# Optimization experiments

Hardware: AMD Instinct MI355X
Metric: run time of the kernel (lower is better)

The kernel has to match this reference:

```python
import jax, jax.numpy as jnp
import numpy as np

D_MODEL = 1024
N_HEAD = 16
D_HEAD = 64
D_CAT = N_HEAD * D_HEAD
HD_MLP = 4096
LN_EPS = 1e-5


def setup_inputs() -> dict:
    key = jax.random.key(0)
    ks = jax.random.split(key, 12)
    bn, t = 2, 2048
    s = lambda fan_in: 1.0 / np.sqrt(fan_in)
    return {
        "x": jax.random.normal(ks[0], (bn, t, D_MODEL), dtype=jnp.float32),
        "mask": jnp.ones((bn, t), dtype=jnp.int32),
        "w_qkv": jax.random.normal(ks[1], (D_MODEL, 3 * D_CAT), dtype=jnp.float32) * s(D_MODEL),
        "w_tail": jax.random.normal(ks[2], (D_CAT, D_MODEL), dtype=jnp.float32) * s(D_CAT),
        "b_tail": jnp.zeros((D_MODEL,), dtype=jnp.float32),
        "ln1_g": jnp.ones((D_MODEL,), dtype=jnp.float32),
        "ln1_b": jnp.zeros((D_MODEL,), dtype=jnp.float32),
        "ln2_g": jnp.ones((D_MODEL,), dtype=jnp.float32),
        "ln2_b": jnp.zeros((D_MODEL,), dtype=jnp.float32),
        "w1": jax.random.normal(ks[3], (D_MODEL, HD_MLP), dtype=jnp.float32) * s(D_MODEL),
        "b1": jnp.zeros((HD_MLP,), dtype=jnp.float32),
        "w2": jax.random.normal(ks[4], (HD_MLP, D_MODEL), dtype=jnp.float32) * s(HD_MLP),
        "b2": jnp.zeros((D_MODEL,), dtype=jnp.float32),
    }


def _layer_norm(x, g, b):
    mu = jnp.mean(x, axis=-1, keepdims=True)
    var = jnp.mean(jnp.square(x - mu), axis=-1, keepdims=True)
    return (x - mu) * jax.lax.rsqrt(var + LN_EPS) * g + b


def _attention(z, mask, w_qkv, w_tail, b_tail):
    bn, t, _ = z.shape
    qkv = z @ w_qkv                      # (bn, t, 3*d_cat)
    qkv = qkv.reshape(bn, t, N_HEAD, 3, D_HEAD)  # chunk layout: per-head [q|k|v]
    q = qkv[..., 0, :].transpose(0, 2, 1, 3)     # (bn, h, t, dh)
    k = qkv[..., 1, :].transpose(0, 2, 1, 3)
    v = qkv[..., 2, :].transpose(0, 2, 1, 3)
    scale = D_HEAD ** -0.5
    dots = jnp.einsum("bhqd,bhkd->bhqk", q, k) * scale
    key_mask = (mask == 0)[:, None, None, :]     # (bn,1,1,t)
    dots = jnp.where(key_mask, -jnp.inf, dots)
    coef = jax.nn.softmax(dots, axis=-1)
    attn = jnp.einsum("bhqk,bhkd->bhqd", coef, v)
    out = attn.transpose(0, 2, 1, 3).reshape(bn, t, D_CAT)
    return out @ w_tail + b_tail


def reference(x, mask, w_qkv, w_tail, b_tail, ln1_g, ln1_b, ln2_g, ln2_b, w1, b1, w2, b2):
    z = _layer_norm(x, ln1_g, ln1_b)
    x = _attention(z, mask, w_qkv, w_tail, b_tail) + x
    z = _layer_norm(x, ln2_g, ln2_b)
    h = jax.nn.gelu(z @ w1 + b1, approximate=False)  # torch GELU default = exact erf
    x = h @ w2 + b2 + x
    return x
```

## Files before the change

kernel.cpp:

```cpp
#include <hip/hip_runtime.h>
#include <hip/hip_bf16.h>

#define DM 1024
#define TT 2048
#define NH 16
#define DH 64
#define HD 4096

typedef __attribute__((ext_vector_type(4))) float f32x4;
typedef __attribute__((ext_vector_type(8))) short s16x8;
typedef __attribute__((ext_vector_type(4))) short s16x4;

static __device__ __forceinline__ short f2bf(float f) {
  __hip_bfloat16 h = __float2bfloat16(f);
  return *reinterpret_cast<short*>(&h);
}

typedef const __attribute__((address_space(1))) char* gas1_t;
typedef __attribute__((address_space(3))) char* las3_t;
static __device__ __forceinline__ void glds16(const void* g, void* l) {
  __builtin_amdgcn_global_load_lds((gas1_t)g, (las3_t)l, 16, 0, 0);
}

__global__ __launch_bounds__(256) void transpose_cvt_k(
    const float* __restrict__ in, short* __restrict__ out, int K, int N)
{
  __shared__ float tile[32][33];
  const int n0 = blockIdx.x * 32, k0 = blockIdx.y * 32;
  const int tx = threadIdx.x & 31, ty = threadIdx.x >> 5;
#pragma unroll
  for (int i = 0; i < 4; ++i)
    tile[ty + i * 8][tx] = in[(size_t)(k0 + ty + i * 8) * N + n0 + tx];
  __syncthreads();
#pragma unroll
  for (int i = 0; i < 4; ++i) {
    int n = ty + i * 8;
    out[(size_t)(n0 + n) * K + k0 + tx] = f2bf(tile[tx][n]);
  }
}

__global__ __launch_bounds__(256) void ln_k(
    const float* __restrict__ x, const float* __restrict__ g,
    const float* __restrict__ b, short* __restrict__ out)
{
  const int row = blockIdx.x;
  const int tid = threadIdx.x;
  const float4 v = ((const float4*)(x + (size_t)row * DM))[tid];
  float s = v.x + v.y + v.z + v.w;
  float q = v.x * v.x + v.y * v.y + v.z * v.z + v.w * v.w;
#pragma unroll
  for (int off = 1; off < 64; off <<= 1) {
    s += __shfl_xor(s, off);
    q += __shfl_xor(q, off);
  }
  __shared__ float ss[4], sq[4];
  const int wave = tid >> 6;
  if ((tid & 63) == 0) { ss[wave] = s; sq[wave] = q; }
  __syncthreads();
  s = ss[0] + ss[1] + ss[2] + ss[3];
  q = sq[0] + sq[1] + sq[2] + sq[3];
  const float mu = s * (1.0f / DM);
  const float var = q * (1.0f / DM) - mu * mu;
  const float rs = rsqrtf(var + 1e-5f);
  const float4 gv = ((const float4*)g)[tid];
  const float4 bv = ((const float4*)b)[tid];
  s16x4 o;
  o[0] = f2bf((v.x - mu) * rs * gv.x + bv.x);
  o[1] = f2bf((v.y - mu) * rs * gv.y + bv.y);
  o[2] = f2bf((v.z - mu) * rs * gv.z + bv.z);
  o[3] = f2bf((v.w - mu) * rs * gv.w + bv.w);
  *(s16x4*)(out + (size_t)row * DM + tid * 4) = o;
}

template<int EPI, int BN>
__global__ __launch_bounds__(256) void gemm_bt(
    const short* __restrict__ A, const short* __restrict__ B,
    const float* __restrict__ bias, const float* __restrict__ res,
    float* __restrict__ outF, short* __restrict__ outB,
    short* __restrict__ outK, short* __restrict__ outV,
    int M, int N, int K)
{
  constexpr int MR = (BN == 128) ? 4 : 2;
  __shared__ short As[2][128 * 32];
  __shared__ short Bs[2][BN * 32];
  const int tid = threadIdx.x;
  const int wave = tid >> 6, lane = tid & 63;
  const int l15 = lane & 15, lhi = lane >> 4;
  const int bm = blockIdx.x, bn = blockIdx.y;
  const int wr = (BN == 128) ? (wave >> 1) : wave;
  const int wc = (BN == 128) ? (wave & 1) : 0;
  f32x4 acc[MR][4] = {};

  const int sr = wave * 16 + (lane >> 2);
  const int schunk = ((lane & 3) ^ ((lane >> 3) & 3)) * 16;
  const char* gA = (const char*)(A + (size_t)(bm * 128 + sr) * K) + schunk;
  const char* gB = (const char*)(B + (size_t)(bn * BN + sr) * K) + schunk;
  const size_t rowstep = (size_t)64 * K * 2;

  const int NK = K >> 5;
  const int rsw = (l15 >> 1) & 3;
  const int achunk = (lhi ^ rsw) << 4;

  auto stage = [&](int buf, int kt) {
    const size_t koff = (size_t)kt * 64;
    char* lA = (char*)As[buf] + wave * 1024;
    glds16(gA + koff, lA);
    glds16(gA + koff + rowstep, lA + 4096);
    char* lB = (char*)Bs[buf] + wave * 1024;
    glds16(gB + koff, lB);
    if (BN == 128) glds16(gB + koff + rowstep, lB + 4096);
  };

  stage(0, 0);
  __syncthreads();
  int cur = 0;
  for (int kt = 0; kt < NK; ++kt) {
    if (kt + 1 < NK) stage(cur ^ 1, kt + 1);
    s16x8 af[MR], bfv[4];
#pragma unroll
    for (int m = 0; m < MR; ++m) {
      const int row = wr * (MR * 16) + m * 16 + l15;
      af[m] = *(const s16x8*)((const char*)As[cur] + row * 64 + achunk);
    }
#pragma unroll
    for (int n = 0; n < 4; ++n) {
      const int row = wc * 64 + n * 16 + l15;
      bfv[n] = *(const s16x8*)((const char*)Bs[cur] + row * 64 + achunk);
    }
#pragma unroll
    for (int m = 0; m < MR; ++m)
#pragma unroll
      for (int n = 0; n < 4; ++n)
        acc[m][n] = __builtin_amdgcn_mfma_f32_16x16x32_bf16(af[m], bfv[n], acc[m][n], 0, 0, 0);
    __syncthreads();
    cur ^= 1;
  }

  const int rowb = bm * 128 + wr * (MR * 16);
  const int colb = bn * BN + wc * 64;
#pragma unroll
  for (int m = 0; m < MR; ++m) {
#pragma unroll
    for (int n = 0; n < 4; ++n) {
      if (EPI == 3) {
        const int col0 = colb + n * 16;
        const int h = col0 / 192;
        const int c0 = col0 - h * 192;
        const int region = c0 >> 6;
        const int d = (c0 & 63) + l15;
        const int row0 = rowb + m * 16 + lhi * 4;
        const int bb = row0 >> 11, tl0 = row0 & 2047;
        const size_t bh = (size_t)bb * NH + h;
        if (region == 2) {
          s16x4 pk;
#pragma unroll
          for (int rr = 0; rr < 4; ++rr) pk[rr] = f2bf(acc[m][n][rr]);
          *(s16x4*)(outV + (bh * 64 + d) * TT + tl0) = pk;
        } else {
          short* dst = (region == 0) ? outB : outK;
#pragma unroll
          for (int rr = 0; rr < 4; ++rr)
            dst[(bh * TT + tl0 + rr) * 64 + d] = f2bf(acc[m][n][rr]);
        }
      } else {
        const int col = colb + n * 16 + l15;
        const float bv = bias[col];
#pragma unroll
        for (int rr = 0; rr < 4; ++rr) {
          const int row = rowb + m * 16 + lhi * 4 + rr;
          float v = acc[m][n][rr] + bv;
          if (EPI == 1) v += res[(size_t)row * N + col];
          if (EPI == 2) v = 0.5f * v * (1.0f + erff(v * 0.70710678118f));
          if (EPI == 1) outF[(size_t)row * N + col] = v;
          else outB[(size_t)row * N + col] = f2bf(v);
        }
      }
    }
  }
}

__global__ __launch_bounds__(256) void attn_k(
    const short* __restrict__ Qb, const short* __restrict__ Kb,
    const short* __restrict__ Vtb, const int* __restrict__ mask,
    short* __restrict__ outp)
{
  const int tid = threadIdx.x, wave = tid >> 6, lane = tid & 63;
  const int l15 = lane & 15, lhi = lane >> 4;
  const int bh = blockIdx.y;
  const int b = bh >> 4, h = bh & 15;
  const int q0 = blockIdx.x * 64;

  __shared__ short Ks[64 * 64];
  __shared__ short Vt[64 * 64];
  __shared__ short Ps[4][16 * 64];

  const short* qbase = Qb + ((size_t)bh * TT + q0 + wave * 16 + l15) * 64;
  const s16x8 aq0 = *(const s16x8*)(qbase + lhi * 8);
  const s16x8 aq1 = *(const s16x8*)(qbase + 32 + lhi * 8);

  f32x4 o[4] = {};
  float mrow = -1e30f, lrow = 0.f;

  const int sr = tid >> 2;
  const int tc = (tid & 3) * 16;
  const int ssw = (sr & 7) << 4;

  const short* kg0 = Kb + ((size_t)bh * TT + sr) * 64 + tc;
  const short* vg0 = Vtb + ((size_t)bh * 64 + sr) * TT + tc;
  s16x8 kr0 = *(const s16x8*)kg0, kr1 = *(const s16x8*)(kg0 + 8);
  s16x8 vr0 = *(const s16x8*)vg0, vr1 = *(const s16x8*)(vg0 + 8);
  int mcur = mask[b * TT + lane];

  for (int t0 = 0; t0 < TT; t0 += 64) {
    char* krow = (char*)Ks + sr * 128;
    *(s16x8*)(krow + ((tc * 2) ^ ssw)) = kr0;
    *(s16x8*)(krow + ((tc * 2 + 16) ^ ssw)) = kr1;
    char* vrow = (char*)Vt + sr * 128;
    *(s16x8*)(vrow + ((tc * 2) ^ ssw)) = vr0;
    *(s16x8*)(vrow + ((tc * 2 + 16) ^ ssw)) = vr1;
    __syncthreads();

    const unsigned long long mb = __ballot(mcur != 0);

    if (t0 + 64 < TT) {
      const short* kg = Kb + ((size_t)bh * TT + t0 + 64 + sr) * 64 + tc;
      const short* vg = Vtb + ((size_t)bh * 64 + sr) * TT + t0 + 64 + tc;
      kr0 = *(const s16x8*)kg; kr1 = *(const s16x8*)(kg + 8);
      vr0 = *(const s16x8*)vg; vr1 = *(const s16x8*)(vg + 8);
      mcur = mask[b * TT + t0 + 64 + lane];
    }

    f32x4 sv[4];
#pragma unroll
    for (int n = 0; n < 4; ++n) {
      const int row = n * 16 + l15;
      const int sw = (row & 7) << 4;
      const char* kr = (const char*)Ks + row * 128;
      const s16x8 a0 = *(const s16x8*)(kr + ((lhi * 16) ^ sw));
      const s16x8 a1 = *(const s16x8*)(kr + ((64 + lhi * 16) ^ sw));
      f32x4 z = {};
      z = __builtin_amdgcn_mfma_f32_16x16x32_bf16(a0, aq0, z, 0, 0, 0);
      z = __builtin_amdgcn_mfma_f32_16x16x32_bf16(a1, aq1, z, 0, 0, 0);
      sv[n] = z;
    }

    float pvv[4][4];
    float mx = -3e38f;
#pragma unroll
    for (int n = 0; n < 4; ++n) {
      const unsigned mnib = (unsigned)(mb >> (n * 16 + lhi * 4)) & 0xF;
#pragma unroll
      for (int r = 0; r < 4; ++r) {
        float val = sv[n][r] * 0.125f;
        if (!((mnib >> r) & 1)) val = -3e38f;
        pvv[n][r] = val;
        mx = fmaxf(mx, val);
      }
    }
    mx = fmaxf(mx, __shfl_xor(mx, 16));
    mx = fmaxf(mx, __shfl_xor(mx, 32));
    const float mn = fmaxf(mrow, mx);
    const float alpha = __expf(mrow - mn);
    mrow = mn;
    float sum = 0.f;
#pragma unroll
    for (int n = 0; n < 4; ++n)
#pragma unroll
      for (int r = 0; r < 4; ++r) {
        const float p = __expf(pvv[n][r] - mn);
        pvv[n][r] = p;
        sum += p;
      }
    sum += __shfl_xor(sum, 16);
    sum += __shfl_xor(sum, 32);
    lrow = lrow * alpha + sum;

    float ar[4];
#pragma unroll
    for (int rr = 0; rr < 4; ++rr) ar[rr] = __shfl(alpha, lhi * 4 + rr);
#pragma unroll
    for (int db = 0; db < 4; ++db)
#pragma unroll
      for (int rr = 0; rr < 4; ++rr) o[db][rr] *= ar[rr];

    char* pbase = (char*)Ps + wave * 2048 + l15 * 128;
    const int swp = (l15 & 7) << 4;
#pragma unroll
    for (int n = 0; n < 4; ++n) {
      s16x4 pk;
#pragma unroll
      for (int r = 0; r < 4; ++r) pk[r] = f2bf(pvv[n][r]);
      *(s16x4*)(pbase + ((n * 32 + lhi * 8) ^ swp)) = pk;
    }
    asm volatile("s_waitcnt lgkmcnt(0)" ::: "memory");
    __builtin_amdgcn_sched_barrier(0);
    const s16x8 ap0 = *(const s16x8*)(pbase + ((lhi * 16) ^ swp));
    const s16x8 ap1 = *(const s16x8*)(pbase + ((64 + lhi * 16) ^ swp));
#pragma unroll
    for (int db = 0; db < 4; ++db) {
      const int vrw = db * 16 + l15;
      const int swv = (vrw & 7) << 4;
      const char* vr = (const char*)Vt + vrw * 128;
      const s16x8 b0 = *(const s16x8*)(vr + ((lhi * 16) ^ swv));
      const s16x8 b1 = *(const s16x8*)(vr + ((64 + lhi * 16) ^ swv));
      o[db] = __builtin_amdgcn_mfma_f32_16x16x32_bf16(ap0, b0, o[db], 0, 0, 0);
      o[db] = __builtin_amdgcn_mfma_f32_16x16x32_bf16(ap1, b1, o[db], 0, 0, 0);
    }
    __syncthreads();
  }

  float lr[4];
#pragma unroll
  for (int rr = 0; rr < 4; ++rr) lr[rr] = __shfl(lrow, lhi * 4 + rr);
#pragma unroll
  for (int db = 0; db < 4; ++db) {
#pragma unroll
    for (int rr = 0; rr < 4; ++rr) {
      const int qg = q0 + wave * 16 + lhi * 4 + rr;
      const int cg = h * 64 + db * 16 + l15;
      outp[(size_t)(b * TT + qg) * DM + cg] = f2bf(o[db][rr] / lr[rr]);
    }
  }
}

extern "C" void kernel_launch(void* const* d_in, const int* in_sizes, int n_in,
                              void* d_out, int out_size, void* d_ws, size_t ws_size,
                              hipStream_t stream)
{
  const float* x      = (const float*)d_in[0];
  const int*   mask   = (const int*)d_in[1];
  const float* w_qkv  = (const float*)d_in[2];
  const float* w_tail = (const float*)d_in[3];
  const float* b_tail = (const float*)d_in[4];
  const float* ln1g   = (const float*)d_in[5];
  const float* ln1b   = (const float*)d_in[6];
  const float* ln2g   = (const float*)d_in[7];
  const float* ln2b   = (const float*)d_in[8];
  const float* w1     = (const float*)d_in[9];
  const float* b1     = (const float*)d_in[10];
  const float* w2     = (const float*)d_in[11];
  const float* b2     = (const float*)d_in[12];

  char* ws = (char*)d_ws;
  size_t off = 0;
  auto take = [&](size_t bytes) {
    char* p = ws + off;
    off += (bytes + 255) & ~(size_t)255;
    return p;
  };
  short* slotW = (short*)take((size_t)4096 * 2048 * 2);
  short* slotZ = (short*)take((size_t)4096 * 1024 * 2);
  short* qb    = (short*)take((size_t)32 * 2048 * 64 * 2);
  short* kb    = (short*)take((size_t)32 * 2048 * 64 * 2);
  short* vtb   = (short*)take((size_t)32 * 64 * 2048 * 2);
  float* x1    = (float*)take((size_t)4096 * 1024 * 4);
  short* hbuf  = (short*)take((size_t)4096 * 4096 * 2);

  transpose_cvt_k<<<dim3(3072 / 32, 1024 / 32), 256, 0, stream>>>(w_qkv, slotW, 1024, 3072);
  ln_k<<<4096, 256, 0, stream>>>(x, ln1g, ln1b, slotZ);
  gemm_bt<3, 128><<<dim3(32, 24), 256, 0, stream>>>(slotZ, slotW, nullptr, nullptr,
                                                    nullptr, qb, kb, vtb, 4096, 3072, 1024);
  attn_k<<<dim3(32, 32), 256, 0, stream>>>(qb, kb, vtb, mask, slotZ);
  transpose_cvt_k<<<dim3(1024 / 32, 1024 / 32), 256, 0, stream>>>(w_tail, slotW, 1024, 1024);
  gemm_bt<1, 64><<<dim3(32, 16), 256, 0, stream>>>(slotZ, slotW, b_tail, x,
                                                   x1, nullptr, nullptr, nullptr, 4096, 1024, 1024);
  ln_k<<<4096, 256, 0, stream>>>(x1, ln2g, ln2b, slotZ);
  transpose_cvt_k<<<dim3(4096 / 32, 1024 / 32), 256, 0, stream>>>(w1, slotW, 1024, 4096);
  gemm_bt<2, 128><<<dim3(32, 32), 256, 0, stream>>>(slotZ, slotW, b1, nullptr,
                                                    nullptr, hbuf, nullptr, nullptr, 4096, 4096, 1024);
  transpose_cvt_k<<<dim3(1024 / 32, 4096 / 32), 256, 0, stream>>>(w2, slotW, 4096, 1024);
  gemm_bt<1, 64><<<dim3(32, 16), 256, 0, stream>>>(hbuf, slotW, b2, x1,
                                                   (float*)d_out, nullptr, nullptr, nullptr, 4096, 1024, 4096);
}
```

Baseline: 299.2 us.

## Widen attention KV tile to 128, fold softmax scale into Q, lazy rescale

The QKV GEMM epilogue now multiplies Q by scale*log2(e) so attention can use exp2f without a per-element scale multiply. The attention kernel processes 128 keys per iteration with doubled shared-memory tiles. It skips mask application when all keys are valid and only rescales the running output when the row max grows by more than a threshold. Blocks are remapped onto a 1D grid to interleave batch-head pairs. The cost is more shared memory and registers per block, which may reduce occupancy, and lazy rescaling leaves exponents less tightly bounded than exact online softmax.

```diff
diff --git a/kernel.cpp b/kernel.cpp
--- a/kernel.cpp
+++ b/kernel.cpp
@@ -158,9 +158,10 @@
           *(s16x4*)(outV + (bh * 64 + d) * TT + tl0) = pk;
         } else {
           short* dst = (region == 0) ? outB : outK;
+          const float qs = (region == 0) ? 0.18033688011112042f : 1.0f;
 #pragma unroll
           for (int rr = 0; rr < 4; ++rr)
-            dst[(bh * TT + tl0 + rr) * 64 + d] = f2bf(acc[m][n][rr]);
+            dst[(bh * TT + tl0 + rr) * 64 + d] = f2bf(acc[m][n][rr] * qs);
         }
       } else {
         const int col = colb + n * 16 + l15;
@@ -186,13 +187,15 @@
 {
   const int tid = threadIdx.x, wave = tid >> 6, lane = tid & 63;
   const int l15 = lane & 15, lhi = lane >> 4;
-  const int bh = blockIdx.y;
+  const int lb = blockIdx.x;
+  const int r = lb & 31;
+  const int bh = (r & 7) * 4 + (r >> 3);
   const int b = bh >> 4, h = bh & 15;
-  const int q0 = blockIdx.x * 64;
-
-  __shared__ short Ks[64 * 64];
-  __shared__ short Vt[64 * 64];
-  __shared__ short Ps[4][16 * 64];
+  const int q0 = (lb >> 5) * 64;
+
+  __shared__ short Ks[128 * 64];
+  __shared__ short Vt[64 * 128];
+  __shared__ short Ps[4][16 * 128];
 
   const short* qbase = Qb + ((size_t)bh * TT + q0 + wave * 16 + l15) * 64;
   const s16x8 aq0 = *(const s16x8*)(qbase + lhi * 8);
@@ -201,38 +204,52 @@
   f32x4 o[4] = {};
   float mrow = -1e30f, lrow = 0.f;
 
-  const int sr = tid >> 2;
-  const int tc = (tid & 3) * 16;
-  const int ssw = (sr & 7) << 4;
-
-  const short* kg0 = Kb + ((size_t)bh * TT + sr) * 64 + tc;
-  const short* vg0 = Vtb + ((size_t)bh * 64 + sr) * TT + tc;
-  s16x8 kr0 = *(const s16x8*)kg0, kr1 = *(const s16x8*)(kg0 + 8);
-  s16x8 vr0 = *(const s16x8*)vg0, vr1 = *(const s16x8*)(vg0 + 8);
-  int mcur = mask[b * TT + lane];
-
-  for (int t0 = 0; t0 < TT; t0 += 64) {
-    char* krow = (char*)Ks + sr * 128;
-    *(s16x8*)(krow + ((tc * 2) ^ ssw)) = kr0;
-    *(s16x8*)(krow + ((tc * 2 + 16) ^ ssw)) = kr1;
-    char* vrow = (char*)Vt + sr * 128;
-    *(s16x8*)(vrow + ((tc * 2) ^ ssw)) = vr0;
-    *(s16x8*)(vrow + ((tc * 2 + 16) ^ ssw)) = vr1;
+  const int kr_s = tid >> 1, kc_s = (tid & 1) * 32;
+  const int ksw = (kr_s & 7) << 4;
+  const int vr_s = tid >> 2, vc_s = (tid & 3) * 32;
+  const int vsw = (vr_s & 7) << 4;
+
+  const short* kgb = Kb + (size_t)bh * TT * 64 + (size_t)kr_s * 64 + kc_s;
+  const short* vgb = Vtb + ((size_t)bh * 64 + vr_s) * TT + vc_s;
+
+  s16x8 kpre[4], vpre[4];
+#pragma unroll
+  for (int j = 0; j < 4; ++j) {
+    kpre[j] = *(const s16x8*)(kgb + j * 8);
+    vpre[j] = *(const s16x8*)(vgb + j * 8);
+  }
+  int m0 = mask[b * TT + lane], m1 = mask[b * TT + 64 + lane];
+
+  for (int t0 = 0; t0 < TT; t0 += 128) {
+    char* krow = (char*)Ks + kr_s * 128;
+#pragma unroll
+    for (int j = 0; j < 4; ++j)
+      *(s16x8*)(krow + ((kc_s * 2 + j * 16) ^ ksw)) = kpre[j];
+    char* vrow = (char*)Vt + vr_s * 256;
+#pragma unroll
+    for (int j = 0; j < 4; ++j)
+      *(s16x8*)(vrow + ((vc_s * 2 + j * 16) ^ vsw)) = vpre[j];
     __syncthreads();
 
-    const unsigned long long mb = __ballot(mcur != 0);
-
-    if (t0 + 64 < TT) {
-      const short* kg = Kb + ((size_t)bh * TT + t0 + 64 + sr) * 64 + tc;
-      const short* vg = Vtb + ((size_t)bh * 64 + sr) * TT + t0 + 64 + tc;
-      kr0 = *(const s16x8*)kg; kr1 = *(const s16x8*)(kg + 8);
-      vr0 = *(const s16x8*)vg; vr1 = *(const s16x8*)(vg + 8);
-      mcur = mask[b * TT + t0 + 64 + lane];
-    }
-
-    f32x4 sv[4];
-#pragma unroll
-    for (int n = 0; n < 4; ++n) {
+    const unsigned long long mb0 = __ballot(m0 != 0);
+    const unsigned long long mb1 = __ballot(m1 != 0);
+    const bool full = (mb0 & mb1) == ~0ULL;
+
+    if (t0 + 128 < TT) {
+      const short* kg = kgb + (size_t)(t0 + 128) * 64;
+      const short* vg = vgb + t0 + 128;
+#pragma unroll
+      for (int j = 0; j < 4; ++j) {
+        kpre[j] = *(const s16x8*)(kg + j * 8);
+        vpre[j] = *(const s16x8*)(vg + j * 8);
+      }
+      m0 = mask[b * TT + t0 + 128 + lane];
+      m1 = mask[b * TT + t0 + 192 + lane];
+    }
+
+    f32x4 sv[8];
+#pragma unroll
+    for (int n = 0; n < 8; ++n) {
       const int row = n * 16 + l15;
       const int sw = (row & 7) << 4;
       const char* kr = (const char*)Ks + row * 128;
@@ -244,67 +261,78 @@
       sv[n] = z;
     }
 
-    float pvv[4][4];
-    float mx = -3e38f;
-#pragma unroll
-    for (int n = 0; n < 4; ++n) {
-      const unsigned mnib = (unsigned)(mb >> (n * 16 + lhi * 4)) & 0xF;
-#pragma unroll
-      for (int r = 0; r < 4; ++r) {
-        float val = sv[n][r] * 0.125f;
-        if (!((mnib >> r) & 1)) val = -3e38f;
-        pvv[n][r] = val;
-        mx = fmaxf(mx, val);
+    if (!full) {
+#pragma unroll
+      for (int n = 0; n < 8; ++n) {
+        const unsigned long long mbn = (n < 4) ? mb0 : mb1;
+        const unsigned nib = (unsigned)(mbn >> ((n & 3) * 16 + lhi * 4)) & 0xF;
+#pragma unroll
+        for (int rr = 0; rr < 4; ++rr)
+          if (!((nib >> rr) & 1)) sv[n][rr] = -3e38f;
       }
     }
+    float mx0 = -3e38f, mx1 = -3e38f, mx2 = -3e38f, mx3 = -3e38f;
+#pragma unroll
+    for (int n = 0; n < 8; ++n) {
+      mx0 = fmaxf(mx0, sv[n][0]); mx1 = fmaxf(mx1, sv[n][1]);
+      mx2 = fmaxf(mx2, sv[n][2]); mx3 = fmaxf(mx3, sv[n][3]);
+    }
+    float mx = fmaxf(fmaxf(mx0, mx1), fmaxf(mx2, mx3));
     mx = fmaxf(mx, __shfl_xor(mx, 16));
     mx = fmaxf(mx, __shfl_xor(mx, 32));
-    const float mn = fmaxf(mrow, mx);
-    const float alpha = __expf(mrow - mn);
-    mrow = mn;
-    float sum = 0.f;
-#pragma unroll
-    for (int n = 0; n < 4; ++n)
-#pragma unroll
-      for (int r = 0; r < 4; ++r) {
-        const float p = __expf(pvv[n][r] - mn);
-        pvv[n][r] = p;
-        sum += p;
-      }
+
+    if (__any(mx > mrow + 8.0f)) {
+      const float mn = fmaxf(mrow, mx);
+      const float alpha = exp2f(mrow - mn);
+      mrow = mn;
+      lrow *= alpha;
+      float ar[4];
+#pragma unroll
+      for (int rr = 0; rr < 4; ++rr) ar[rr] = __shfl(alpha, lhi * 4 + rr);
+#pragma unroll
+      for (int db = 0; db < 4; ++db)
+#pragma unroll
+        for (int rr = 0; rr < 4; ++rr) o[db][rr] *= ar[rr];
+    }
+
+    float s0 = 0.f, s1 = 0.f, s2 = 0.f, s3 = 0.f;
+#pragma unroll
+    for (int n = 0; n < 8; ++n) {
+      sv[n][0] = exp2f(sv[n][0] - mrow); s0 += sv[n][0];
+      sv[n][1] = exp2f(sv[n][1] - mrow); s1 += sv[n][1];
+      sv[n][2] = exp2f(sv[n][2] - mrow); s2 += sv[n][2];
+      sv[n][3] = exp2f(sv[n][3] - mrow); s3 += sv[n][3];
+    }
+    float sum = (s0 + s1) + (s2 + s3);
     sum += __shfl_xor(sum, 16);
     sum += __shfl_xor(sum, 32);
-    lrow = lrow * alpha + sum;
-
-    float ar[4];
-#pragma unroll
-    for (int rr = 0; rr < 4; ++rr) ar[rr] = __shfl(alpha, lhi * 4 + rr);
-#pragma unroll
-    for (int db = 0; db < 4; ++db)
-#pragma unroll
-      for (int rr = 0; rr < 4; ++rr) o[db][rr] *= ar[rr];
-
-    char* pbase = (char*)Ps + wave * 2048 + l15 * 128;
+    lrow += sum;
+
+    char* pbase = (char*)Ps + wave * 4096 + l15 * 256;
     const int swp = (l15 & 7) << 4;
 #pragma unroll
-    for (int n = 0; n < 4; ++n) {
+    for (int n = 0; n < 8; ++n) {
       s16x4 pk;
 #pragma unroll
-      for (int r = 0; r < 4; ++r) pk[r] = f2bf(pvv[n][r]);
+      for (int rr = 0; rr < 4; ++rr) pk[rr] = f2bf(sv[n][rr]);
       *(s16x4*)(pbase + ((n * 32 + lhi * 8) ^ swp)) = pk;
     }
     asm volatile("s_waitcnt lgkmcnt(0)" ::: "memory");
     __builtin_amdgcn_sched_barrier(0);
-    const s16x8 ap0 = *(const s16x8*)(pbase + ((lhi * 16) ^ swp));
-    const s16x8 ap1 = *(const s16x8*)(pbase + ((64 + lhi * 16) ^ swp));
+    s16x8 ap[4];
+#pragma unroll
+    for (int ks = 0; ks < 4; ++ks)
+      ap[ks] = *(const s16x8*)(pbase + ((ks * 64 + lhi * 16) ^ swp));
 #pragma unroll
     for (int db = 0; db < 4; ++db) {
-      const int vrw = db * 16 + l15;
-      const int swv = (vrw & 7) << 4;
-      const char* vr = (const char*)Vt + vrw * 128;
-      const s16x8 b0 = *(const s16x8*)(vr + ((lhi * 16) ^ swv));
-      const s16x8 b1 = *(const s16x8*)(vr + ((64 + lhi * 16) ^ swv));
-      o[db] = __builtin_amdgcn_mfma_f32_16x16x32_bf16(ap0, b0, o[db], 0, 0, 0);
-      o[db] = __builtin_amdgcn_mfma_f32_16x16x32_bf16(ap1, b1, o[db], 0, 0, 0);
+      const int d = db * 16 + l15;
+      const int swv = (d & 7) << 4;
+      const char* vr2 = (const char*)Vt + d * 256;
+#pragma unroll
+      for (int ks = 0; ks < 4; ++ks) {
+        const s16x8 bv = *(const s16x8*)(vr2 + ((ks * 64 + lhi * 16) ^ swv));
+        o[db] = __builtin_amdgcn_mfma_f32_16x16x32_bf16(ap[ks], bv, o[db], 0, 0, 0);
+      }
     }
     __syncthreads();
   }
@@ -360,7 +388,7 @@
   ln_k<<<4096, 256, 0, stream>>>(x, ln1g, ln1b, slotZ);
   gemm_bt<3, 128><<<dim3(32, 24), 256, 0, stream>>>(slotZ, slotW, nullptr, nullptr,
                                                     nullptr, qb, kb, vtb, 4096, 3072, 1024);
-  attn_k<<<dim3(32, 32), 256, 0, stream>>>(qb, kb, vtb, mask, slotZ);
+  attn_k<<<1024, 256, 0, stream>>>(qb, kb, vtb, mask, slotZ);
   transpose_cvt_k<<<dim3(1024 / 32, 1024 / 32), 256, 0, stream>>>(w_tail, slotW, 1024, 1024);
   gemm_bt<1, 64><<<dim3(32, 16), 256, 0, stream>>>(slotZ, slotW, b_tail, x,
                                                    x1, nullptr, nullptr, nullptr, 4096, 1024, 1024);
```

Result: no change. 294.3 us (-1.6%).
